# Performance work log

Hardware: AMD Instinct MI355X
Metric: run time of the kernel (lower is better)

Reference implementation:

```python
import jax, jax.numpy as jnp
import numpy as np
from jax import lax

B, C, H, W = 4096, 10, 30, 30
NCOL = C - 1                      # non-background colors 1..9
_pi, _pj = np.triu_indices(NCOL, 1)  # lexicographic (i<j) pair order, matches the python double loop
PI = jnp.asarray(_pi); PJ = jnp.asarray(_pj)
NPAIR = int(_pi.shape[0])         # 36
W_TRANSFORM, W_EXACT, W_AFFINE, W_ROT, W_REFL, W_GEO, W_EDGE, W_CBAL = 0.2, 7.0, 0.4, 0.3, 0.3, 0.5, 0.3, 0.2
GAMMA = 1.4


def setup_inputs() -> dict:
    key = jax.random.key(0)
    ks = jax.random.split(key, 6)
    pred = jax.random.normal(ks[0], (B, C, H, W), jnp.float32)
    tidx = jax.random.randint(ks[1], (B, H, W), 0, C)
    target = jnp.transpose(jax.nn.one_hot(tidx, C, dtype=jnp.float32), (0, 3, 1, 2))
    iidx = jax.random.randint(ks[2], (B, H, W), 0, C)
    input_grid = jnp.transpose(jax.nn.one_hot(iidx, C, dtype=jnp.float32), (0, 3, 1, 2))
    theta = 0.1 * jax.random.normal(ks[3], (B, 2, 3), jnp.float32)
    rot = jax.random.normal(ks[4], (B, 8), jnp.float32)
    refl = jax.random.normal(ks[5], (B, 4), jnp.float32)
    return {"pred_output": pred, "target_output": target, "input_grid": input_grid,
            "theta": theta, "rotation_logits": rot, "reflection_logits": refl}


def _detect_edges(idx):
    # idx: [B,H,W] int; pixel is an edge if it differs from any h/w neighbor
    dh = idx[:, 1:, :] != idx[:, :-1, :]
    dw = idx[:, :, 1:] != idx[:, :, :-1]
    e = jnp.pad(dh, ((0, 0), (1, 0), (0, 0))) | jnp.pad(dh, ((0, 0), (0, 1), (0, 0)))
    e = e | jnp.pad(dw, ((0, 0), (0, 0), (1, 0))) | jnp.pad(dw, ((0, 0), (0, 0), (0, 1)))
    return e


def _entropy_mean(logits):
    lp = jax.nn.log_softmax(logits, axis=1)
    return (-(jnp.exp(lp) * lp).sum(axis=1)).mean()


def _sobel(idx_f):
    sx = jnp.array([[-1., 0., 1.], [-2., 0., 2.], [-1., 0., 1.]], jnp.float32).reshape(1, 1, 3, 3)
    sy = jnp.array([[-1., -2., -1.], [0., 0., 0.], [1., 2., 1.]], jnp.float32).reshape(1, 1, 3, 3)
    x = idx_f[:, None]  # [B,1,H,W]
    dn = ('NCHW', 'OIHW', 'NCHW')
    ex = lax.conv_general_dilated(x, sx, (1, 1), ((1, 1), (1, 1)), dimension_numbers=dn)
    ey = lax.conv_general_dilated(x, sy, (1, 1), ((1, 1), (1, 1)), dimension_numbers=dn)
    return jnp.sqrt(ex * ex + ey * ey)


def _centers(grid):
    # grid: [H,W] int -> per-color (1..9) center of mass and presence
    cols = jnp.arange(1, C)
    mask = (grid[None] == cols[:, None, None]).astype(jnp.float32)  # [9,H,W]
    cnt = mask.sum((1, 2))
    ys = jnp.arange(H, dtype=jnp.float32)[:, None]
    xs = jnp.arange(W, dtype=jnp.float32)[None, :]
    cy = (mask * ys).sum((1, 2)) / jnp.maximum(cnt, 1.0)
    cx = (mask * xs).sum((1, 2)) / jnp.maximum(cnt, 1.0)
    return cy, cx, cnt > 0


def _compact_dists(cy, cx, present):
    # distances for all 36 color pairs, compacted so valid pairs occupy
    # the leading slots in the same lexicographic order as the torch loops
    d = jnp.sqrt((cy[PI] - cy[PJ]) ** 2 + (cx[PI] - cx[PJ]) ** 2)
    v = present[PI] & present[PJ]
    rank = jnp.cumsum(v.astype(jnp.int32)) - 1
    slot = jnp.where(v, rank, NPAIR)          # dump invalid pairs in scratch slot
    compact = jnp.zeros(NPAIR + 1, jnp.float32).at[slot].set(d)
    return compact[:NPAIR], v.sum()


def _geo_sample(pidx, tidx):
    cyp, cxp, prp = _centers(pidx)
    cyt, cxt, prt = _centers(tidx)
    dp, n_p = _compact_dists(cyp, cxp, prp)
    dt, n_t = _compact_dists(cyt, cxt, prt)
    m = jnp.minimum(n_p, n_t)                 # min_len truncation
    use = jnp.arange(NPAIR) < m
    sq = jnp.where(use, (dp - dt) ** 2, 0.0)
    return jnp.where(m > 0, sq.sum() / jnp.maximum(m, 1).astype(jnp.float32), 0.0)


def _components(pred, target, inp, theta, rot, refl):
    tidx = jnp.argmax(target, axis=1)
    pidx = jnp.argmax(pred, axis=1)
    iidx = jnp.argmax(inp, axis=1)
    # spatial focal CE with edge-weighted pixels
    lp = jax.nn.log_softmax(pred, axis=1)
    ce = -jnp.take_along_axis(lp, tidx[:, None], axis=1)[:, 0]  # [B,H,W]
    pt = jnp.exp(-ce)
    sw = jnp.where(_detect_edges(tidx), 1.5, 1.0)
    spatial_focal = ((1.0 - pt) ** GAMMA * ce * sw).mean()
    # exact match bonus / copy penalty
    exact = jnp.all(pidx == tidx, axis=(1, 2)).astype(jnp.float32)
    exact_count = exact.sum()
    exact_bonus = -exact.mean() * W_EXACT
    copy = jnp.all(pidx == iidx, axis=(1, 2)).astype(jnp.float32)
    transform = copy.mean() * W_TRANSFORM
    # affine regularization on theta
    scale_reg = jnp.sqrt((theta[:, :2, :2] ** 2).sum((1, 2)))
    trans_reg = jnp.sqrt((theta[:, :, 2] ** 2).sum(1))
    affine = (scale_reg.mean() + 0.1 * trans_reg.mean()) * W_AFFINE
    rotation = _entropy_mean(rot) * W_ROT
    reflection = _entropy_mean(refl) * W_REFL
    # geometric color-center consistency (vmapped over batch)
    geo = jax.vmap(_geo_sample)(pidx, tidx).sum() / B * W_GEO
    # sobel edge MSE on argmax indices
    pe = _sobel(pidx.astype(jnp.float32))
    te = _sobel(tidx.astype(jnp.float32))
    edge = jnp.mean((pe - te) ** 2) * W_EDGE
    # color balance
    pc = jax.nn.softmax(pred, axis=1).sum((2, 3))
    tc = target.sum((2, 3))
    pc = pc / (pc.sum(1, keepdims=True) + 1e-8)
    tc = tc / (tc.sum(1, keepdims=True) + 1e-8)
    cbal = jnp.mean((pc - tc) ** 2) * W_CBAL
    total = (spatial_focal + transform + affine + rotation + reflection
             + geo + edge + cbal + exact_bonus)
    return (total, spatial_focal, transform, exact_bonus, exact_count,
            affine, rotation, reflection, geo, edge, cbal)


def reference(pred_output, target_output, input_grid, theta, rotation_logits, reflection_logits):
    return _components(pred_output, target_output, input_grid, theta,
                       rotation_logits, reflection_logits)
```

## Files before the change

### kernel.cpp

```cpp
#include <hip/hip_runtime.h>
#include <stdint.h>

#define B_   4096
#define C_   10
#define H_   30
#define W_   30
#define HW_  900
#define NCOL_ 9
#define NPART 9


__device__ __forceinline__ float entropyN(const float* __restrict__ x, int n) {
    float m = x[0];
    for (int i = 1; i < n; ++i) m = fmaxf(m, x[i]);
    float se = 0.f;
    for (int i = 0; i < n; ++i) se += __expf(x[i] - m);
    float lse = m + __logf(se);
    float ent = 0.f;
    for (int i = 0; i < n; ++i) { float lp = x[i] - lse; ent -= __expf(lp) * lp; }
    return ent;
}


__global__ __launch_bounds__(64) void zero_out_k(float* out, int n) {
    int i = threadIdx.x;
    if (i < n) out[i] = 0.f;
}

__global__ __launch_bounds__(256, 4) void loss_main(
    const float* __restrict__ pred, const float* __restrict__ target,
    const float* __restrict__ inp,  const float* __restrict__ theta,
    const float* __restrict__ rotl, const float* __restrict__ refl,
    float* __restrict__ partials ,
    float* __restrict__ out)
{
    __shared__ uint8_t s_t[33 * 32];
    __shared__ uint8_t s_p[33 * 32];
    __shared__ __align__(16) float s_cef[30 * 36];
    __shared__ unsigned long long s_ctr[2][NCOL_];
    __shared__ float s_wred[4][16];
    __shared__ float s_dp[36], s_dt[36];
    __shared__ float s_cy[2][NCOL_], s_cx[2][NCOL_];
    __shared__ int   s_pr[2][NCOL_];
    __shared__ int   s_tcnt[NCOL_];
    __shared__ float s_small[4];

    const int t = threadIdx.x;
    const int b = blockIdx.x;
    const size_t base = (size_t)b * (C_ * HW_);

    float pc[C_];
#pragma unroll
    for (int c = 0; c < C_; ++c) pc[c] = 0.f;
    float exact_f = 1.f, copy_f = 1.f;

    if (t < 225) {
        const int p0 = 4 * t;
        const float* pp = pred   + base + p0;
        const float* tp = target + base + p0;
        const float* gp = inp    + base + p0;

        float4 pfv[C_];
#pragma unroll
        for (int c = 0; c < C_; ++c)
            pfv[c] = *reinterpret_cast<const float4*>(pp + c * HW_);
        float4 tfv[C_];
#pragma unroll
        for (int c = 0; c < C_; ++c)
            tfv[c] = *reinterpret_cast<const float4*>(tp + c * HW_);

        float vt[4]  = {0.f, 0.f, 0.f, 0.f};
        float tif[4] = {0.f, 0.f, 0.f, 0.f};
        float iif[4] = {0.f, 0.f, 0.f, 0.f};
#pragma unroll
        for (int c = 0; c < C_; ++c) {
            float4 gf = *reinterpret_cast<const float4*>(gp + c * HW_);
            const float4 tf = tfv[c];
            const float4 pf = pfv[c];
            const float fc = (float)c;
            vt[0] = fmaf(tf.x, pf.x, vt[0]); vt[1] = fmaf(tf.y, pf.y, vt[1]);
            vt[2] = fmaf(tf.z, pf.z, vt[2]); vt[3] = fmaf(tf.w, pf.w, vt[3]);
            tif[0] = fmaf(tf.x, fc, tif[0]); tif[1] = fmaf(tf.y, fc, tif[1]);
            tif[2] = fmaf(tf.z, fc, tif[2]); tif[3] = fmaf(tf.w, fc, tif[3]);
            iif[0] = fmaf(gf.x, fc, iif[0]); iif[1] = fmaf(gf.y, fc, iif[1]);
            iif[2] = fmaf(gf.z, fc, iif[2]); iif[3] = fmaf(gf.w, fc, iif[3]);
        }

        int h = p0 / 30;
        int w = p0 - 30 * h;
#pragma unroll
        for (int j = 0; j < 4; ++j) {
            const int ti = (int)tif[j];
            const int ii = (int)iif[j];
            const float* pj = (const float*)&pfv[0];
            float pm = pj[j]; int pi = 0;
            float se = 0.f;
            float ex[C_];
#pragma unroll
            for (int c = 0; c < C_; ++c) {
                const float raw = ((const float*)&pfv[c])[j];
                if (c > 0 && raw > pm) { pm = raw; pi = c; }
                float e = __expf(raw);
                ex[c] = e;
                se += e;
            }
            const float inv = __builtin_amdgcn_rcpf(se);
#pragma unroll
            for (int c = 0; c < C_; ++c) pc[c] = fmaf(ex[c], inv, pc[c]);
            const float ce = __logf(se) - vt[j];

            s_t[(h + 1) * 32 + (w + 1)] = (uint8_t)ti;
            s_p[(h + 1) * 32 + (w + 1)] = (uint8_t)pi;
            s_cef[36 * h + w] = ce;
            if (pi != ti) exact_f = 0.f;
            if (pi != ii) copy_f = 0.f;
            if (++w == 30) { w = 0; ++h; }
        }
    } else if (t < 252) {
        const int z = t - 225;
        for (int k = z; k < 32; k += 27) {
            const int g = k >> 4, r = (k >> 3) & 1, dw = k & 7;
            uint32_t* pb = (uint32_t*)((g ? s_p : s_t) + (r ? 31 * 32 : 0));
            pb[dw] = 0u;
        }
        for (int k = z; k < 120; k += 27) {
            const int g = (k >= 60);
            const int kk = k - 60 * g;
            const int r = 1 + (kk >> 1);
            const int cp = (kk & 1) ? 31 : 0;
            (g ? s_p : s_t)[r * 32 + cp] = 0;
        }
        for (int k = z; k < 2 * NCOL_; k += 27) ((unsigned long long*)s_ctr)[k] = 0ull;
    } else if (t == 252) {
        s_small[0] = entropyN(rotl + (size_t)b * 8, 8);
    } else if (t == 253) {
        s_small[1] = entropyN(refl + (size_t)b * 4, 4);
    } else if (t == 254) {
        const float* th = theta + (size_t)b * 6;
        float sreg = sqrtf(th[0]*th[0] + th[1]*th[1] + th[3]*th[3] + th[4]*th[4]);
        float treg = sqrtf(th[2]*th[2] + th[5]*th[5]);
        s_small[2] = sreg + 0.1f * treg;
    }
    __syncthreads();

    float focal = 0.f, edg = 0.f;
    if (t < 240) {
        const int h = t >> 3, wq = t & 7;
        const int w0 = 4 * wq;
        const int npx = (w0 < 28) ? 4 : 2;

        const uint32_t* tr0 = (const uint32_t*)(s_t + 32 * h);
        const uint32_t* tr1 = (const uint32_t*)(s_t + 32 * (h + 1));
        const uint32_t* tr2 = (const uint32_t*)(s_t + 32 * (h + 2));
        const uint32_t* pr0 = (const uint32_t*)(s_p + 32 * h);
        const uint32_t* pr1 = (const uint32_t*)(s_p + 32 * (h + 1));
        const uint32_t* pr2 = (const uint32_t*)(s_p + 32 * (h + 2));

        uint32_t td[3][2] = {{tr0[wq], tr0[wq + 1]}, {tr1[wq], tr1[wq + 1]}, {tr2[wq], tr2[wq + 1]}};
        uint32_t pd[3][2] = {{pr0[wq], pr0[wq + 1]}, {pr1[wq], pr1[wq + 1]}, {pr2[wq], pr2[wq + 1]}};
        const float4 cef = *reinterpret_cast<const float4*>(s_cef + 36 * h + w0);
        const float cearr[4] = {cef.x, cef.y, cef.z, cef.w};

        int tb[3][6], pb[3][6];
#pragma unroll
        for (int r = 0; r < 3; ++r) {
            const uint32_t d0t = td[r][0], d1t = td[r][1];
            tb[r][0] = d0t & 255; tb[r][1] = (d0t >> 8) & 255; tb[r][2] = (d0t >> 16) & 255;
            tb[r][3] = d0t >> 24; tb[r][4] = d1t & 255; tb[r][5] = (d1t >> 8) & 255;
            const uint32_t d0p = pd[r][0], d1p = pd[r][1];
            pb[r][0] = d0p & 255; pb[r][1] = (d0p >> 8) & 255; pb[r][2] = (d0p >> 16) & 255;
            pb[r][3] = d0p >> 24; pb[r][4] = d1p & 255; pb[r][5] = (d1p >> 8) & 255;
        }
        int s1t[6], s2t[6], s1p[6], s2p[6];
#pragma unroll
        for (int j = 0; j < 6; ++j) {
            s1t[j] = tb[0][j] + 2 * tb[1][j] + tb[2][j];
            s2t[j] = tb[2][j] - tb[0][j];
            s1p[j] = pb[0][j] + 2 * pb[1][j] + pb[2][j];
            s2p[j] = pb[2][j] - pb[0][j];
        }
#pragma unroll
        for (int k = 0; k < 4; ++k) {
            if (k < npx) {
                const int w = w0 + k;
                const int tv = tb[1][k + 1], pv = pb[1][k + 1];
                const bool eg = (h > 0  && tb[0][k + 1] != tv) ||
                                (h < 29 && tb[2][k + 1] != tv) ||
                                (w > 0  && tb[1][k]     != tv) ||
                                (w < 29 && tb[1][k + 2] != tv);
                const float ce = cearr[k];
                const float pt = __expf(-ce);
                const float omt = fmaxf(1.f - pt, 0.f);
                focal += __powf(omt, 1.4f) * ce * (eg ? 1.5f : 1.0f);

                const int ext = s1t[k + 2] - s1t[k];
                const int eyt = s2t[k] + 2 * s2t[k + 1] + s2t[k + 2];
                const int exq = s1p[k + 2] - s1p[k];
                const int eyq = s2p[k] + 2 * s2p[k + 1] + s2p[k + 2];
                const float mt = sqrtf((float)(ext * ext + eyt * eyt));
                const float mp = sqrtf((float)(exq * exq + eyq * eyq));
                const float dd = mp - mt;
                edg += dd * dd;

                const unsigned long long add =
                    (1ull << 42) | ((unsigned long long)(unsigned)h << 21) | (unsigned)w;
                if (tv > 0) atomicAdd(&s_ctr[1][tv - 1], add);
                if (pv > 0) atomicAdd(&s_ctr[0][pv - 1], add);
            }
        }
    }

    float vals[14];
    vals[0] = focal; vals[1] = edg;
#pragma unroll
    for (int c = 0; c < C_; ++c) vals[2 + c] = pc[c];
    vals[12] = exact_f; vals[13] = copy_f;
#pragma unroll
    for (int off = 32; off > 0; off >>= 1) {
#pragma unroll
        for (int k = 0; k < 12; ++k) vals[k] += __shfl_down(vals[k], off);
        vals[12] = fminf(vals[12], __shfl_down(vals[12], off));
        vals[13] = fminf(vals[13], __shfl_down(vals[13], off));
    }
    const int wid = t >> 6, lane = t & 63;
    if (lane == 0) {
#pragma unroll
        for (int k = 0; k < 14; ++k) s_wred[wid][k] = vals[k];
    }
    __syncthreads();

    if (t < 18) {
        const int g = (t >= 9);
        const int k = t - 9 * g;
        const unsigned long long q = s_ctr[g][k];
        const int sx = (int)(q & 0x1FFFFF), sy = (int)((q >> 21) & 0x1FFFFF), cn = (int)(q >> 42);
        const float dn = fmaxf((float)cn, 1.f);
        s_cy[g][k] = (float)sy / dn;
        s_cx[g][k] = (float)sx / dn;
        s_pr[g][k] = (cn > 0);
        if (g) s_tcnt[k] = cn;
    }
    __syncthreads();

    if (t < 64) {
        const int l = t;
        const int i = (l >= 8) + (l >= 15) + (l >= 21) + (l >= 26) +
                      (l >= 30) + (l >= 33) + (l >= 35);
        const int j = l - (i * (17 - i)) / 2 + i + 1;
        bool vp = false, vtp = false;
        float dp = 0.f, dt = 0.f;
        if (l < 36) {
            vp  = s_pr[0][i] && s_pr[0][j];
            vtp = s_pr[1][i] && s_pr[1][j];
            float dyp = s_cy[0][i] - s_cy[0][j], dxp = s_cx[0][i] - s_cx[0][j];
            dp = sqrtf(dyp * dyp + dxp * dxp);
            float dyt = s_cy[1][i] - s_cy[1][j], dxt = s_cx[1][i] - s_cx[1][j];
            dt = sqrtf(dyt * dyt + dxt * dxt);
        }
        const unsigned long long mp_mask = __ballot(vp);
        const unsigned long long mt_mask = __ballot(vtp);
        const unsigned long long below = (1ull << l) - 1ull;
        if (vp)  s_dp[__popcll(mp_mask & below)] = dp;
        if (vtp) s_dt[__popcll(mt_mask & below)] = dt;
        const int np = (int)__popcll(mp_mask);
        const int nt = (int)__popcll(mt_mask);
        const int mm = np < nt ? np : nt;
        float term = 0.f;
        if (l < mm) { float d = s_dp[l] - s_dt[l]; term = d * d; }
#pragma unroll
        for (int off = 32; off > 0; off >>= 1) term += __shfl_down(term, off);

        if (t == 0) {
            const float geo_b = (mm > 0) ? term / (float)mm : 0.f;

            float r[14];
#pragma unroll
            for (int k = 0; k < 14; ++k) r[k] = s_wred[0][k];
            for (int w2 = 1; w2 < 4; ++w2) {
#pragma unroll
                for (int k = 0; k < 12; ++k) r[k] += s_wred[w2][k];
                r[12] = fminf(r[12], s_wred[w2][12]);
                r[13] = fminf(r[13], s_wred[w2][13]);
            }

            float pcs = 0.f;
#pragma unroll
            for (int c = 0; c < C_; ++c) pcs += r[2 + c];
            const float ipcs = 1.f / (pcs + 1e-8f);
            int tsum = 0;
#pragma unroll
            for (int k = 0; k < NCOL_; ++k) tsum += s_tcnt[k];
            float cb = 0.f;
            const float itd = 1.f / (900.f + 1e-8f);
            {
                float d = r[2] * ipcs - (float)(HW_ - tsum) * itd;
                cb += d * d;
            }
#pragma unroll
            for (int c = 1; c < C_; ++c) {
                float d = r[2 + c] * ipcs - (float)s_tcnt[c - 1] * itd;
                cb += d * d;
            }

            float res[NPART];
            res[0] = r[0];
            res[1] = r[12];
            res[2] = r[13];
            res[3] = s_small[2];
            res[4] = s_small[0];
            res[5] = s_small[1];
            res[6] = geo_b;
            res[7] = r[1];
            res[8] = cb;

            if (partials) {
                float* pw = partials + (size_t)b * NPART;
#pragma unroll
                for (int k = 0; k < NPART; ++k) pw[k] = res[k];
            } else {
                atomicAdd(&out[1],  res[0]);
                atomicAdd(&out[2],  res[2]);
                atomicAdd(&out[4],  res[1]);
                atomicAdd(&out[5],  res[3]);
                atomicAdd(&out[6],  res[4]);
                atomicAdd(&out[7],  res[5]);
                atomicAdd(&out[8],  res[6]);
                atomicAdd(&out[9],  res[7]);
                atomicAdd(&out[10], res[8]);
            }
        }
    }
}

__device__ __forceinline__ void write_final(float* out,
    double focal_s, double exact_s, double copy_s, double aff_s,
    double rot_s, double refl_s, double geo_s, double edge_s, double cbal_s)
{
    const double invB = 1.0 / (double)B_;
    float focal      = (float)(focal_s / ((double)B_ * (double)HW_));
    float transform  = (float)(copy_s * invB * 0.2);
    float exact_cnt  = (float)exact_s;
    float exact_bns  = (float)(-(exact_s * invB) * 7.0);
    float affine     = (float)(aff_s * invB * 0.4);
    float rotation   = (float)(rot_s * invB * 0.3);
    float reflection = (float)(refl_s * invB * 0.3);
    float geo        = (float)(geo_s * invB * 0.5);
    float edge       = (float)(edge_s / ((double)B_ * (double)HW_) * 0.3);
    float cbal       = (float)(cbal_s / ((double)B_ * (double)C_) * 0.2);
    out[0] = focal + transform + affine + rotation + reflection + geo + edge + cbal + exact_bns;
    out[1] = focal; out[2] = transform; out[3] = exact_bns; out[4] = exact_cnt;
    out[5] = affine; out[6] = rotation; out[7] = reflection; out[8] = geo;
    out[9] = edge; out[10] = cbal;
}

__global__ __launch_bounds__(256) void reduce_partials(
    const float* __restrict__ partials, float* __restrict__ out)
{
    __shared__ double sh[256][NPART];
    const int t = threadIdx.x;
    double acc[NPART];
#pragma unroll
    for (int k = 0; k < NPART; ++k) acc[k] = 0.0;
    for (int b = t; b < B_; b += 256) {
        const float* pp = partials + (size_t)b * NPART;
#pragma unroll
        for (int k = 0; k < NPART; ++k) acc[k] += (double)pp[k];
    }
#pragma unroll
    for (int k = 0; k < NPART; ++k) sh[t][k] = acc[k];
    __syncthreads();
    for (int s = 128; s > 0; s >>= 1) {
        if (t < s) {
#pragma unroll
            for (int k = 0; k < NPART; ++k) sh[t][k] += sh[t + s][k];
        }
        __syncthreads();
    }
    if (t == 0) {
        write_final(out, sh[0][0], sh[0][1], sh[0][2], sh[0][3],
                    sh[0][4], sh[0][5], sh[0][6], sh[0][7], sh[0][8]);
    }
}

__global__ void finalize_atomic(float* out) {
    if (threadIdx.x == 0) {
        write_final(out, (double)out[1], (double)out[4], (double)out[2], (double)out[5],
                    (double)out[6], (double)out[7], (double)out[8], (double)out[9],
                    (double)out[10]);
    }
}


extern "C" void kernel_launch(void* const* d_in, const int* in_sizes, int n_in,
                              void* d_out, int out_size, void* d_ws, size_t ws_size,
                              hipStream_t stream) {
    const float* pred   = (const float*)d_in[0];
    const float* target = (const float*)d_in[1];
    const float* inp    = (const float*)d_in[2];
    const float* theta  = (const float*)d_in[3];
    const float* rotl   = (const float*)d_in[4];
    const float* refl   = (const float*)d_in[5];
    float* out = (float*)d_out;

    const size_t need = (size_t)B_ * NPART * sizeof(float);
    if (d_ws != nullptr && ws_size >= need) {
        loss_main<<<B_, 256, 0, stream>>>(pred, target, inp, theta, rotl, refl,
                                          (float*)d_ws, out);
        reduce_partials<<<1, 256, 0, stream>>>((const float*)d_ws, out);
    } else {
        zero_out_k<<<1, 64, 0, stream>>>(out, out_size);
        loss_main<<<B_, 256, 0, stream>>>(pred, target, inp, theta, rotl, refl,
                                          nullptr, out);
        finalize_atomic<<<1, 1, 0, stream>>>(out);
    }
}
```

Before: 94.75 us.

## Process one batch sample per wavefront instead of per block

Remaps the loss kernel so each 64-lane wavefront handles one sample, with four samples per 256-thread block. All block-wide __syncthreads are replaced by wave-local LDS fences, exact and copy flags become wave votes, and the cross-wave shared-memory reduction is dropped. Focal weighting is also precomputed per pixel in the first pass, so the edge pass only adds the extra half weight on edge pixels. Each wave now loops over four chunks of pixels serially, which lowers memory-level parallelism per sample and raises LDS use per block in exchange for removing block barriers.

Measured after the change: 98.55 us. +4.0%, slower.

```diff
diff --git a/kernel.cpp b/kernel.cpp
--- a/kernel.cpp
+++ b/kernel.cpp
@@ -8,6 +8,7 @@
 #define HW_  900
 #define NCOL_ 9
 #define NPART 9
+#define WVB  4
 
 
 __device__ __forceinline__ float entropyN(const float* __restrict__ x, int n) {
@@ -21,6 +22,12 @@
     return ent;
 }
 
+__device__ __forceinline__ void wave_fence_lds() {
+    asm volatile("s_waitcnt lgkmcnt(0)" ::: "memory");
+    __builtin_amdgcn_wave_barrier();
+    __builtin_amdgcn_sched_barrier(0);
+}
+
 
 __global__ __launch_bounds__(64) void zero_out_k(float* out, int n) {
     int i = threadIdx.x;
@@ -34,132 +41,130 @@
     float* __restrict__ partials ,
     float* __restrict__ out)
 {
-    __shared__ uint8_t s_t[33 * 32];
-    __shared__ uint8_t s_p[33 * 32];
-    __shared__ __align__(16) float s_cef[30 * 36];
-    __shared__ unsigned long long s_ctr[2][NCOL_];
-    __shared__ float s_wred[4][16];
-    __shared__ float s_dp[36], s_dt[36];
-    __shared__ float s_cy[2][NCOL_], s_cx[2][NCOL_];
-    __shared__ int   s_pr[2][NCOL_];
-    __shared__ int   s_tcnt[NCOL_];
-    __shared__ float s_small[4];
-
-    const int t = threadIdx.x;
-    const int b = blockIdx.x;
+    __shared__ uint8_t s_t[WVB][33 * 32];
+    __shared__ uint8_t s_p[WVB][33 * 32];
+    __shared__ __align__(16) float s_fb[WVB][30 * 36];
+    __shared__ unsigned long long s_ctr[WVB][2][NCOL_];
+    __shared__ float s_cy[WVB][2][NCOL_], s_cx[WVB][2][NCOL_];
+    __shared__ int   s_pr[WVB][2][NCOL_];
+    __shared__ int   s_tcnt[WVB][NCOL_];
+    __shared__ float s_dp[WVB][36], s_dt[WVB][36];
+    __shared__ float s_small[WVB][4];
+
+    const int t    = threadIdx.x;
+    const int wv   = t >> 6;
+    const int lane = t & 63;
+    const int b    = blockIdx.x * WVB + wv;
     const size_t base = (size_t)b * (C_ * HW_);
 
+    uint8_t* st = s_t[wv];
+    uint8_t* sp = s_p[wv];
+    float*   sfb = s_fb[wv];
+
+    {
+        uint32_t* zt = (uint32_t*)st;
+        uint32_t* zp = (uint32_t*)sp;
+#pragma unroll 1
+        for (int k = lane; k < 264; k += 64) { zt[k] = 0u; zp[k] = 0u; }
+        if (lane < 2 * NCOL_) ((unsigned long long*)s_ctr[wv])[lane] = 0ull;
+    }
+    wave_fence_lds();
+
     float pc[C_];
 #pragma unroll
     for (int c = 0; c < C_; ++c) pc[c] = 0.f;
-    float exact_f = 1.f, copy_f = 1.f;
-
-    if (t < 225) {
-        const int p0 = 4 * t;
-        const float* pp = pred   + base + p0;
-        const float* tp = target + base + p0;
-        const float* gp = inp    + base + p0;
-
-        float4 pfv[C_];
-#pragma unroll
-        for (int c = 0; c < C_; ++c)
-            pfv[c] = *reinterpret_cast<const float4*>(pp + c * HW_);
-        float4 tfv[C_];
-#pragma unroll
-        for (int c = 0; c < C_; ++c)
-            tfv[c] = *reinterpret_cast<const float4*>(tp + c * HW_);
-
-        float vt[4]  = {0.f, 0.f, 0.f, 0.f};
-        float tif[4] = {0.f, 0.f, 0.f, 0.f};
-        float iif[4] = {0.f, 0.f, 0.f, 0.f};
-#pragma unroll
-        for (int c = 0; c < C_; ++c) {
-            float4 gf = *reinterpret_cast<const float4*>(gp + c * HW_);
-            const float4 tf = tfv[c];
-            const float4 pf = pfv[c];
-            const float fc = (float)c;
-            vt[0] = fmaf(tf.x, pf.x, vt[0]); vt[1] = fmaf(tf.y, pf.y, vt[1]);
-            vt[2] = fmaf(tf.z, pf.z, vt[2]); vt[3] = fmaf(tf.w, pf.w, vt[3]);
-            tif[0] = fmaf(tf.x, fc, tif[0]); tif[1] = fmaf(tf.y, fc, tif[1]);
-            tif[2] = fmaf(tf.z, fc, tif[2]); tif[3] = fmaf(tf.w, fc, tif[3]);
-            iif[0] = fmaf(gf.x, fc, iif[0]); iif[1] = fmaf(gf.y, fc, iif[1]);
-            iif[2] = fmaf(gf.z, fc, iif[2]); iif[3] = fmaf(gf.w, fc, iif[3]);
-        }
-
-        int h = p0 / 30;
-        int w = p0 - 30 * h;
-#pragma unroll
-        for (int j = 0; j < 4; ++j) {
-            const int ti = (int)tif[j];
-            const int ii = (int)iif[j];
-            const float* pj = (const float*)&pfv[0];
-            float pm = pj[j]; int pi = 0;
-            float se = 0.f;
-            float ex[C_];
+    float focal_base = 0.f;
+    bool ok_e = true, ok_c = true;
+
+#pragma unroll 1
+    for (int it = 0; it < 4; ++it) {
+        const int p0 = 256 * it + 4 * lane;
+        if (p0 < HW_) {
+            const float* pp = pred   + base + p0;
+            const float* tp = target + base + p0;
+            const float* gp = inp    + base + p0;
+
+            float4 pfv[C_];
+#pragma unroll
+            for (int c = 0; c < C_; ++c)
+                pfv[c] = *reinterpret_cast<const float4*>(pp + c * HW_);
+            float4 tfv[C_];
+#pragma unroll
+            for (int c = 0; c < C_; ++c)
+                tfv[c] = *reinterpret_cast<const float4*>(tp + c * HW_);
+
+            float vt[4]  = {0.f, 0.f, 0.f, 0.f};
+            float tif[4] = {0.f, 0.f, 0.f, 0.f};
+            float iif[4] = {0.f, 0.f, 0.f, 0.f};
 #pragma unroll
             for (int c = 0; c < C_; ++c) {
-                const float raw = ((const float*)&pfv[c])[j];
-                if (c > 0 && raw > pm) { pm = raw; pi = c; }
-                float e = __expf(raw);
-                ex[c] = e;
-                se += e;
+                float4 gf = *reinterpret_cast<const float4*>(gp + c * HW_);
+                const float4 tf = tfv[c];
+                const float4 pf = pfv[c];
+                const float fc = (float)c;
+                vt[0] = fmaf(tf.x, pf.x, vt[0]); vt[1] = fmaf(tf.y, pf.y, vt[1]);
+                vt[2] = fmaf(tf.z, pf.z, vt[2]); vt[3] = fmaf(tf.w, pf.w, vt[3]);
+                tif[0] = fmaf(tf.x, fc, tif[0]); tif[1] = fmaf(tf.y, fc, tif[1]);
+                tif[2] = fmaf(tf.z, fc, tif[2]); tif[3] = fmaf(tf.w, fc, tif[3]);
+                iif[0] = fmaf(gf.x, fc, iif[0]); iif[1] = fmaf(gf.y, fc, iif[1]);
+                iif[2] = fmaf(gf.z, fc, iif[2]); iif[3] = fmaf(gf.w, fc, iif[3]);
             }
-            const float inv = __builtin_amdgcn_rcpf(se);
-#pragma unroll
-            for (int c = 0; c < C_; ++c) pc[c] = fmaf(ex[c], inv, pc[c]);
-            const float ce = __logf(se) - vt[j];
-
-            s_t[(h + 1) * 32 + (w + 1)] = (uint8_t)ti;
-            s_p[(h + 1) * 32 + (w + 1)] = (uint8_t)pi;
-            s_cef[36 * h + w] = ce;
-            if (pi != ti) exact_f = 0.f;
-            if (pi != ii) copy_f = 0.f;
-            if (++w == 30) { w = 0; ++h; }
-        }
-    } else if (t < 252) {
-        const int z = t - 225;
-        for (int k = z; k < 32; k += 27) {
-            const int g = k >> 4, r = (k >> 3) & 1, dw = k & 7;
-            uint32_t* pb = (uint32_t*)((g ? s_p : s_t) + (r ? 31 * 32 : 0));
-            pb[dw] = 0u;
-        }
-        for (int k = z; k < 120; k += 27) {
-            const int g = (k >= 60);
-            const int kk = k - 60 * g;
-            const int r = 1 + (kk >> 1);
-            const int cp = (kk & 1) ? 31 : 0;
-            (g ? s_p : s_t)[r * 32 + cp] = 0;
-        }
-        for (int k = z; k < 2 * NCOL_; k += 27) ((unsigned long long*)s_ctr)[k] = 0ull;
-    } else if (t == 252) {
-        s_small[0] = entropyN(rotl + (size_t)b * 8, 8);
-    } else if (t == 253) {
-        s_small[1] = entropyN(refl + (size_t)b * 4, 4);
-    } else if (t == 254) {
-        const float* th = theta + (size_t)b * 6;
-        float sreg = sqrtf(th[0]*th[0] + th[1]*th[1] + th[3]*th[3] + th[4]*th[4]);
-        float treg = sqrtf(th[2]*th[2] + th[5]*th[5]);
-        s_small[2] = sreg + 0.1f * treg;
-    }
-    __syncthreads();
-
-    float focal = 0.f, edg = 0.f;
-    if (t < 240) {
-        const int h = t >> 3, wq = t & 7;
+
+            int h = p0 / 30;
+            int w = p0 - 30 * h;
+#pragma unroll
+            for (int j = 0; j < 4; ++j) {
+                const int ti = (int)tif[j];
+                const int ii = (int)iif[j];
+                float pm = ((const float*)&pfv[0])[j]; int pi = 0;
+                float se = 0.f;
+                float ex[C_];
+#pragma unroll
+                for (int c = 0; c < C_; ++c) {
+                    const float raw = ((const float*)&pfv[c])[j];
+                    if (c > 0 && raw > pm) { pm = raw; pi = c; }
+                    float e = __expf(raw);
+                    ex[c] = e;
+                    se += e;
+                }
+                const float inv = __builtin_amdgcn_rcpf(se);
+#pragma unroll
+                for (int c = 0; c < C_; ++c) pc[c] = fmaf(ex[c], inv, pc[c]);
+                const float ce = __logf(se) - vt[j];
+                const float pt = __expf(-ce);
+                const float omt = fmaxf(1.f - pt, 0.f);
+                const float fb = __powf(omt, 1.4f) * ce;
+                focal_base += fb;
+
+                st[(h + 1) * 32 + (w + 1)] = (uint8_t)ti;
+                sp[(h + 1) * 32 + (w + 1)] = (uint8_t)pi;
+                sfb[36 * h + w] = fb;
+                if (pi != ti) ok_e = false;
+                if (pi != ii) ok_c = false;
+                if (++w == 30) { w = 0; ++h; }
+            }
+        }
+    }
+    wave_fence_lds();
+
+    float edg = 0.f, focal_edge = 0.f;
+#pragma unroll 1
+    for (int s = lane; s < 240; s += 64) {
+        const int h = s >> 3, wq = s & 7;
         const int w0 = 4 * wq;
         const int npx = (w0 < 28) ? 4 : 2;
 
-        const uint32_t* tr0 = (const uint32_t*)(s_t + 32 * h);
-        const uint32_t* tr1 = (const uint32_t*)(s_t + 32 * (h + 1));
-        const uint32_t* tr2 = (const uint32_t*)(s_t + 32 * (h + 2));
-        const uint32_t* pr0 = (const uint32_t*)(s_p + 32 * h);
-        const uint32_t* pr1 = (const uint32_t*)(s_p + 32 * (h + 1));
-        const uint32_t* pr2 = (const uint32_t*)(s_p + 32 * (h + 2));
+        const uint32_t* tr0 = (const uint32_t*)(st + 32 * h);
+        const uint32_t* tr1 = (const uint32_t*)(st + 32 * (h + 1));
+        const uint32_t* tr2 = (const uint32_t*)(st + 32 * (h + 2));
+        const uint32_t* pr0 = (const uint32_t*)(sp + 32 * h);
+        const uint32_t* pr1 = (const uint32_t*)(sp + 32 * (h + 1));
+        const uint32_t* pr2 = (const uint32_t*)(sp + 32 * (h + 2));
 
         uint32_t td[3][2] = {{tr0[wq], tr0[wq + 1]}, {tr1[wq], tr1[wq + 1]}, {tr2[wq], tr2[wq + 1]}};
         uint32_t pd[3][2] = {{pr0[wq], pr0[wq + 1]}, {pr1[wq], pr1[wq + 1]}, {pr2[wq], pr2[wq + 1]}};
-        const float4 cef = *reinterpret_cast<const float4*>(s_cef + 36 * h + w0);
-        const float cearr[4] = {cef.x, cef.y, cef.z, cef.w};
+        const float4 fbf = *reinterpret_cast<const float4*>(sfb + 36 * h + w0);
+        const float fbarr[4] = {fbf.x, fbf.y, fbf.z, fbf.w};
 
         int tb[3][6], pb[3][6];
 #pragma unroll
@@ -188,10 +193,7 @@
                                 (h < 29 && tb[2][k + 1] != tv) ||
                                 (w > 0  && tb[1][k]     != tv) ||
                                 (w < 29 && tb[1][k + 2] != tv);
-                const float ce = cearr[k];
-                const float pt = __expf(-ce);
-                const float omt = fmaxf(1.f - pt, 0.f);
-                focal += __powf(omt, 1.4f) * ce * (eg ? 1.5f : 1.0f);
+                if (eg) focal_edge += fbarr[k];
 
                 const int ext = s1t[k + 2] - s1t[k];
                 const int eyt = s2t[k] + 2 * s2t[k + 1] + s2t[k + 2];
@@ -204,130 +206,125 @@
 
                 const unsigned long long add =
                     (1ull << 42) | ((unsigned long long)(unsigned)h << 21) | (unsigned)w;
-                if (tv > 0) atomicAdd(&s_ctr[1][tv - 1], add);
-                if (pv > 0) atomicAdd(&s_ctr[0][pv - 1], add);
+                if (tv > 0) atomicAdd(&s_ctr[wv][1][tv - 1], add);
+                if (pv > 0) atomicAdd(&s_ctr[wv][0][pv - 1], add);
             }
         }
     }
 
-    float vals[14];
-    vals[0] = focal; vals[1] = edg;
+    float vals[12];
+    vals[0] = focal_base + 0.5f * focal_edge;
+    vals[1] = edg;
 #pragma unroll
     for (int c = 0; c < C_; ++c) vals[2 + c] = pc[c];
-    vals[12] = exact_f; vals[13] = copy_f;
 #pragma unroll
     for (int off = 32; off > 0; off >>= 1) {
 #pragma unroll
         for (int k = 0; k < 12; ++k) vals[k] += __shfl_down(vals[k], off);
-        vals[12] = fminf(vals[12], __shfl_down(vals[12], off));
-        vals[13] = fminf(vals[13], __shfl_down(vals[13], off));
-    }
-    const int wid = t >> 6, lane = t & 63;
-    if (lane == 0) {
-#pragma unroll
-        for (int k = 0; k < 14; ++k) s_wred[wid][k] = vals[k];
-    }
-    __syncthreads();
-
-    if (t < 18) {
-        const int g = (t >= 9);
-        const int k = t - 9 * g;
-        const unsigned long long q = s_ctr[g][k];
+    }
+    const float exact_f = __all(ok_e) ? 1.f : 0.f;
+    const float copy_f  = __all(ok_c) ? 1.f : 0.f;
+
+    if (lane == 1)      s_small[wv][0] = entropyN(rotl + (size_t)b * 8, 8);
+    else if (lane == 2) s_small[wv][1] = entropyN(refl + (size_t)b * 4, 4);
+    else if (lane == 3) {
+        const float* th = theta + (size_t)b * 6;
+        float sreg = sqrtf(th[0]*th[0] + th[1]*th[1] + th[3]*th[3] + th[4]*th[4]);
+        float treg = sqrtf(th[2]*th[2] + th[5]*th[5]);
+        s_small[wv][2] = sreg + 0.1f * treg;
+    }
+
+    wave_fence_lds();
+    if (lane < 18) {
+        const int g = (lane >= 9);
+        const int k = lane - 9 * g;
+        const unsigned long long q = s_ctr[wv][g][k];
         const int sx = (int)(q & 0x1FFFFF), sy = (int)((q >> 21) & 0x1FFFFF), cn = (int)(q >> 42);
         const float dn = fmaxf((float)cn, 1.f);
-        s_cy[g][k] = (float)sy / dn;
-        s_cx[g][k] = (float)sx / dn;
-        s_pr[g][k] = (cn > 0);
-        if (g) s_tcnt[k] = cn;
-    }
-    __syncthreads();
-
-    if (t < 64) {
-        const int l = t;
-        const int i = (l >= 8) + (l >= 15) + (l >= 21) + (l >= 26) +
-                      (l >= 30) + (l >= 33) + (l >= 35);
-        const int j = l - (i * (17 - i)) / 2 + i + 1;
-        bool vp = false, vtp = false;
-        float dp = 0.f, dt = 0.f;
-        if (l < 36) {
-            vp  = s_pr[0][i] && s_pr[0][j];
-            vtp = s_pr[1][i] && s_pr[1][j];
-            float dyp = s_cy[0][i] - s_cy[0][j], dxp = s_cx[0][i] - s_cx[0][j];
-            dp = sqrtf(dyp * dyp + dxp * dxp);
-            float dyt = s_cy[1][i] - s_cy[1][j], dxt = s_cx[1][i] - s_cx[1][j];
-            dt = sqrtf(dyt * dyt + dxt * dxt);
-        }
-        const unsigned long long mp_mask = __ballot(vp);
-        const unsigned long long mt_mask = __ballot(vtp);
-        const unsigned long long below = (1ull << l) - 1ull;
-        if (vp)  s_dp[__popcll(mp_mask & below)] = dp;
-        if (vtp) s_dt[__popcll(mt_mask & below)] = dt;
-        const int np = (int)__popcll(mp_mask);
-        const int nt = (int)__popcll(mt_mask);
-        const int mm = np < nt ? np : nt;
-        float term = 0.f;
-        if (l < mm) { float d = s_dp[l] - s_dt[l]; term = d * d; }
-#pragma unroll
-        for (int off = 32; off > 0; off >>= 1) term += __shfl_down(term, off);
-
-        if (t == 0) {
-            const float geo_b = (mm > 0) ? term / (float)mm : 0.f;
-
-            float r[14];
-#pragma unroll
-            for (int k = 0; k < 14; ++k) r[k] = s_wred[0][k];
-            for (int w2 = 1; w2 < 4; ++w2) {
-#pragma unroll
-                for (int k = 0; k < 12; ++k) r[k] += s_wred[w2][k];
-                r[12] = fminf(r[12], s_wred[w2][12]);
-                r[13] = fminf(r[13], s_wred[w2][13]);
-            }
-
-            float pcs = 0.f;
-#pragma unroll
-            for (int c = 0; c < C_; ++c) pcs += r[2 + c];
-            const float ipcs = 1.f / (pcs + 1e-8f);
-            int tsum = 0;
-#pragma unroll
-            for (int k = 0; k < NCOL_; ++k) tsum += s_tcnt[k];
-            float cb = 0.f;
-            const float itd = 1.f / (900.f + 1e-8f);
-            {
-                float d = r[2] * ipcs - (float)(HW_ - tsum) * itd;
-                cb += d * d;
-            }
-#pragma unroll
-            for (int c = 1; c < C_; ++c) {
-                float d = r[2 + c] * ipcs - (float)s_tcnt[c - 1] * itd;
-                cb += d * d;
-            }
-
-            float res[NPART];
-            res[0] = r[0];
-            res[1] = r[12];
-            res[2] = r[13];
-            res[3] = s_small[2];
-            res[4] = s_small[0];
-            res[5] = s_small[1];
-            res[6] = geo_b;
-            res[7] = r[1];
-            res[8] = cb;
-
-            if (partials) {
-                float* pw = partials + (size_t)b * NPART;
-#pragma unroll
-                for (int k = 0; k < NPART; ++k) pw[k] = res[k];
-            } else {
-                atomicAdd(&out[1],  res[0]);
-                atomicAdd(&out[2],  res[2]);
-                atomicAdd(&out[4],  res[1]);
-                atomicAdd(&out[5],  res[3]);
-                atomicAdd(&out[6],  res[4]);
-                atomicAdd(&out[7],  res[5]);
-                atomicAdd(&out[8],  res[6]);
-                atomicAdd(&out[9],  res[7]);
-                atomicAdd(&out[10], res[8]);
-            }
+        s_cy[wv][g][k] = (float)sy / dn;
+        s_cx[wv][g][k] = (float)sx / dn;
+        s_pr[wv][g][k] = (cn > 0);
+        if (g) s_tcnt[wv][k] = cn;
+    }
+    wave_fence_lds();
+
+    const int l = lane;
+    const int i = (l >= 8) + (l >= 15) + (l >= 21) + (l >= 26) +
+                  (l >= 30) + (l >= 33) + (l >= 35);
+    const int j = l - (i * (17 - i)) / 2 + i + 1;
+    bool vp = false, vtp = false;
+    float dp = 0.f, dt = 0.f;
+    if (l < 36) {
+        vp  = s_pr[wv][0][i] && s_pr[wv][0][j];
+        vtp = s_pr[wv][1][i] && s_pr[wv][1][j];
+        float dyp = s_cy[wv][0][i] - s_cy[wv][0][j], dxp = s_cx[wv][0][i] - s_cx[wv][0][j];
+        dp = sqrtf(dyp * dyp + dxp * dxp);
+        float dyt = s_cy[wv][1][i] - s_cy[wv][1][j], dxt = s_cx[wv][1][i] - s_cx[wv][1][j];
+        dt = sqrtf(dyt * dyt + dxt * dxt);
+    }
+    const unsigned long long mp_mask = __ballot(vp);
+    const unsigned long long mt_mask = __ballot(vtp);
+    const unsigned long long below = (1ull << l) - 1ull;
+    if (vp)  s_dp[wv][__popcll(mp_mask & below)] = dp;
+    if (vtp) s_dt[wv][__popcll(mt_mask & below)] = dt;
+    const int np = (int)__popcll(mp_mask);
+    const int nt = (int)__popcll(mt_mask);
+    const int mm = np < nt ? np : nt;
+    wave_fence_lds();
+    float term = 0.f;
+    if (l < mm) { float d = s_dp[wv][l] - s_dt[wv][l]; term = d * d; }
+#pragma unroll
+    for (int off = 32; off > 0; off >>= 1) term += __shfl_down(term, off);
+
+    wave_fence_lds();
+
+    if (lane == 0) {
+        const float geo_b = (mm > 0) ? term / (float)mm : 0.f;
+
+        float pcs = 0.f;
+#pragma unroll
+        for (int c = 0; c < C_; ++c) pcs += vals[2 + c];
+        const float ipcs = 1.f / (pcs + 1e-8f);
+        int tsum = 0;
+#pragma unroll
+        for (int k = 0; k < NCOL_; ++k) tsum += s_tcnt[wv][k];
+        float cb = 0.f;
+        const float itd = 1.f / (900.f + 1e-8f);
+        {
+            float d = vals[2] * ipcs - (float)(HW_ - tsum) * itd;
+            cb += d * d;
+        }
+#pragma unroll
+        for (int c = 1; c < C_; ++c) {
+            float d = vals[2 + c] * ipcs - (float)s_tcnt[wv][c - 1] * itd;
+            cb += d * d;
+        }
+
+        float res[NPART];
+        res[0] = vals[0];
+        res[1] = exact_f;
+        res[2] = copy_f;
+        res[3] = s_small[wv][2];
+        res[4] = s_small[wv][0];
+        res[5] = s_small[wv][1];
+        res[6] = geo_b;
+        res[7] = vals[1];
+        res[8] = cb;
+
+        if (partials) {
+            float* pw = partials + (size_t)b * NPART;
+#pragma unroll
+            for (int k = 0; k < NPART; ++k) pw[k] = res[k];
+        } else {
+            atomicAdd(&out[1],  res[0]);
+            atomicAdd(&out[2],  res[2]);
+            atomicAdd(&out[4],  res[1]);
+            atomicAdd(&out[5],  res[3]);
+            atomicAdd(&out[6],  res[4]);
+            atomicAdd(&out[7],  res[5]);
+            atomicAdd(&out[8],  res[6]);
+            atomicAdd(&out[9],  res[7]);
+            atomicAdd(&out[10], res[8]);
         }
     }
 }
@@ -404,13 +401,13 @@
 
     const size_t need = (size_t)B_ * NPART * sizeof(float);
     if (d_ws != nullptr && ws_size >= need) {
-        loss_main<<<B_, 256, 0, stream>>>(pred, target, inp, theta, rotl, refl,
-                                          (float*)d_ws, out);
+        loss_main<<<B_ / WVB, 256, 0, stream>>>(pred, target, inp, theta, rotl, refl,
+                                                (float*)d_ws, out);
         reduce_partials<<<1, 256, 0, stream>>>((const float*)d_ws, out);
     } else {
         zero_out_k<<<1, 64, 0, stream>>>(out, out_size);
-        loss_main<<<B_, 256, 0, stream>>>(pred, target, inp, theta, rotl, refl,
-                                          nullptr, out);
+        loss_main<<<B_ / WVB, 256, 0, stream>>>(pred, target, inp, theta, rotl, refl,
+                                                nullptr, out);
         finalize_atomic<<<1, 1, 0, stream>>>(out);
     }
 }
```

## Stage inputs through double-buffered async global-to-LDS loads in pixel tiles

Applied to the files above, without the earlier changes.

Replaces the per-thread float4 register loads of pred, target and input with a four-tile loop. Each tile is copied straight into a double-buffered shared-memory area with global_load_lds, and explicit vmcnt waits and barriers let the next tile's copy overlap the current tile's softmax and argmax work. The focal base term now runs in the first phase, and the edge pass adds only the extra 0.5 weight for edge pixels. The aim is to overlap memory traffic with compute, but the new staging buffer takes about 60KB of LDS per block, which can lower occupancy on a kernel that is already close to its bandwidth limit.

Result: slower. 134.7 us (+42.2%).

```diff
diff --git a/kernel.cpp b/kernel.cpp
--- a/kernel.cpp
+++ b/kernel.cpp
@@ -8,6 +8,11 @@
 #define HW_  900
 #define NCOL_ 9
 #define NPART 9
+#define TILE 256
+#define NT   4
+
+#define AS1 __attribute__((address_space(1)))
+#define AS3 __attribute__((address_space(3)))
 
 
 __device__ __forceinline__ float entropyN(const float* __restrict__ x, int n) {
@@ -34,9 +39,10 @@
     float* __restrict__ partials ,
     float* __restrict__ out)
 {
+    __shared__ float s_buf[2][3][C_][TILE];
     __shared__ uint8_t s_t[33 * 32];
     __shared__ uint8_t s_p[33 * 32];
-    __shared__ __align__(16) float s_cef[30 * 36];
+    __shared__ __align__(16) float s_fb[30 * 36];
     __shared__ unsigned long long s_ctr[2][NCOL_];
     __shared__ float s_wred[4][16];
     __shared__ float s_dp[36], s_dt[36];
@@ -45,61 +51,79 @@
     __shared__ int   s_tcnt[NCOL_];
     __shared__ float s_small[4];
 
-    const int t = threadIdx.x;
-    const int b = blockIdx.x;
+    const int t    = threadIdx.x;
+    const int wid  = t >> 6;
+    const int lane = t & 63;
+    const int b    = blockIdx.x;
     const size_t base = (size_t)b * (C_ * HW_);
 
+    {
+        uint32_t* zt = (uint32_t*)s_t;
+        uint32_t* zp = (uint32_t*)s_p;
+        for (int k = t; k < 264; k += 256) { zt[k] = 0u; zp[k] = 0u; }
+        if (t < 2 * NCOL_) ((unsigned long long*)s_ctr)[t] = 0ull;
+    }
+    __syncthreads();
+
+    const size_t LIM = (size_t)B_ * C_ * HW_ - 4;
+    auto stage = [&](int tb, int tile, bool clampT) {
+        const size_t toff = base + (size_t)tile * TILE + 4 * (size_t)lane;
+#pragma unroll 1
+        for (int ch = wid; ch < C_; ch += 4) {
+            size_t idx = toff + (size_t)ch * HW_;
+            if (clampT && idx > LIM) idx = LIM;
+            __builtin_amdgcn_global_load_lds((const AS1 void*)(pred + idx),
+                                             (AS3 void*)&s_buf[tb][0][ch][0], 16, 0, 0);
+            __builtin_amdgcn_global_load_lds((const AS1 void*)(target + idx),
+                                             (AS3 void*)&s_buf[tb][1][ch][0], 16, 0, 0);
+            __builtin_amdgcn_global_load_lds((const AS1 void*)(inp + idx),
+                                             (AS3 void*)&s_buf[tb][2][ch][0], 16, 0, 0);
+        }
+    };
+
     float pc[C_];
 #pragma unroll
     for (int c = 0; c < C_; ++c) pc[c] = 0.f;
-    float exact_f = 1.f, copy_f = 1.f;
-
-    if (t < 225) {
-        const int p0 = 4 * t;
-        const float* pp = pred   + base + p0;
-        const float* tp = target + base + p0;
-        const float* gp = inp    + base + p0;
-
-        float4 pfv[C_];
-#pragma unroll
-        for (int c = 0; c < C_; ++c)
-            pfv[c] = *reinterpret_cast<const float4*>(pp + c * HW_);
-        float4 tfv[C_];
-#pragma unroll
-        for (int c = 0; c < C_; ++c)
-            tfv[c] = *reinterpret_cast<const float4*>(tp + c * HW_);
-
-        float vt[4]  = {0.f, 0.f, 0.f, 0.f};
-        float tif[4] = {0.f, 0.f, 0.f, 0.f};
-        float iif[4] = {0.f, 0.f, 0.f, 0.f};
-#pragma unroll
-        for (int c = 0; c < C_; ++c) {
-            float4 gf = *reinterpret_cast<const float4*>(gp + c * HW_);
-            const float4 tf = tfv[c];
-            const float4 pf = pfv[c];
-            const float fc = (float)c;
-            vt[0] = fmaf(tf.x, pf.x, vt[0]); vt[1] = fmaf(tf.y, pf.y, vt[1]);
-            vt[2] = fmaf(tf.z, pf.z, vt[2]); vt[3] = fmaf(tf.w, pf.w, vt[3]);
-            tif[0] = fmaf(tf.x, fc, tif[0]); tif[1] = fmaf(tf.y, fc, tif[1]);
-            tif[2] = fmaf(tf.z, fc, tif[2]); tif[3] = fmaf(tf.w, fc, tif[3]);
-            iif[0] = fmaf(gf.x, fc, iif[0]); iif[1] = fmaf(gf.y, fc, iif[1]);
-            iif[2] = fmaf(gf.z, fc, iif[2]); iif[3] = fmaf(gf.w, fc, iif[3]);
-        }
-
-        int h = p0 / 30;
-        int w = p0 - 30 * h;
-#pragma unroll
-        for (int j = 0; j < 4; ++j) {
-            const int ti = (int)tif[j];
-            const int ii = (int)iif[j];
-            const float* pj = (const float*)&pfv[0];
-            float pm = pj[j]; int pi = 0;
-            float se = 0.f;
+    float focal_base = 0.f;
+    bool ok_e = true, ok_c = true;
+
+    stage(0, 0, false);
+#pragma unroll 1
+    for (int tt = 0; tt < NT; ++tt) {
+        const int tb = tt & 1;
+        if (tt + 1 < NT) {
+            stage(tb ^ 1, tt + 1, (tt + 1 == NT - 1));
+            if (wid < 2) asm volatile("s_waitcnt vmcnt(9)" ::: "memory");
+            else         asm volatile("s_waitcnt vmcnt(6)" ::: "memory");
+        } else {
+            asm volatile("s_waitcnt vmcnt(0)" ::: "memory");
+        }
+        __builtin_amdgcn_s_barrier();
+        asm volatile("" ::: "memory");
+
+        const int px = tt * TILE + t;
+        if (px < HW_) {
+            const float* bp  = &s_buf[tb][0][0][t];
+            const float* btg = &s_buf[tb][1][0][t];
+            const float* big = &s_buf[tb][2][0][t];
+            float tif = 0.f, iif = 0.f;
+            float pv[C_];
+#pragma unroll
+            for (int c = 0; c < C_; ++c) {
+                pv[c] = bp[c * TILE];
+                tif = fmaf(btg[c * TILE], (float)c, tif);
+                iif = fmaf(big[c * TILE], (float)c, iif);
+            }
+            const int ti = (int)tif;
+            const int ii = (int)iif;
+            float pm = pv[0]; int pi = 0;
+            float se = 0.f, vt = pv[0];
             float ex[C_];
 #pragma unroll
             for (int c = 0; c < C_; ++c) {
-                const float raw = ((const float*)&pfv[c])[j];
+                const float raw = pv[c];
                 if (c > 0 && raw > pm) { pm = raw; pi = c; }
+                if (c == ti) vt = raw;
                 float e = __expf(raw);
                 ex[c] = e;
                 se += e;
@@ -107,30 +131,86 @@
             const float inv = __builtin_amdgcn_rcpf(se);
 #pragma unroll
             for (int c = 0; c < C_; ++c) pc[c] = fmaf(ex[c], inv, pc[c]);
-            const float ce = __logf(se) - vt[j];
-
+            const float ce = __logf(se) - vt;
+            const float pt = __expf(-ce);
+            const float omt = fmaxf(1.f - pt, 0.f);
+            const float fb = __powf(omt, 1.4f) * ce;
+            focal_base += fb;
+
+            const int h = px / 30, w = px - 30 * h;
             s_t[(h + 1) * 32 + (w + 1)] = (uint8_t)ti;
             s_p[(h + 1) * 32 + (w + 1)] = (uint8_t)pi;
-            s_cef[36 * h + w] = ce;
-            if (pi != ti) exact_f = 0.f;
-            if (pi != ii) copy_f = 0.f;
-            if (++w == 30) { w = 0; ++h; }
-        }
-    } else if (t < 252) {
-        const int z = t - 225;
-        for (int k = z; k < 32; k += 27) {
-            const int g = k >> 4, r = (k >> 3) & 1, dw = k & 7;
-            uint32_t* pb = (uint32_t*)((g ? s_p : s_t) + (r ? 31 * 32 : 0));
-            pb[dw] = 0u;
-        }
-        for (int k = z; k < 120; k += 27) {
-            const int g = (k >= 60);
-            const int kk = k - 60 * g;
-            const int r = 1 + (kk >> 1);
-            const int cp = (kk & 1) ? 31 : 0;
-            (g ? s_p : s_t)[r * 32 + cp] = 0;
-        }
-        for (int k = z; k < 2 * NCOL_; k += 27) ((unsigned long long*)s_ctr)[k] = 0ull;
+            s_fb[36 * h + w] = fb;
+            if (pi != ti) ok_e = false;
+            if (pi != ii) ok_c = false;
+        }
+        asm volatile("s_waitcnt lgkmcnt(0)" ::: "memory");
+        __builtin_amdgcn_s_barrier();
+        asm volatile("" ::: "memory");
+    }
+
+    float focal_edge = 0.f, edg = 0.f;
+    if (t < 240) {
+        const int h = t >> 3, wq = t & 7;
+        const int w0 = 4 * wq;
+        const int npx = (w0 < 28) ? 4 : 2;
+
+        const uint32_t* tr0 = (const uint32_t*)(s_t + 32 * h);
+        const uint32_t* tr1 = (const uint32_t*)(s_t + 32 * (h + 1));
+        const uint32_t* tr2 = (const uint32_t*)(s_t + 32 * (h + 2));
+        const uint32_t* pr0 = (const uint32_t*)(s_p + 32 * h);
+        const uint32_t* pr1 = (const uint32_t*)(s_p + 32 * (h + 1));
+        const uint32_t* pr2 = (const uint32_t*)(s_p + 32 * (h + 2));
+
+        uint32_t td[3][2] = {{tr0[wq], tr0[wq + 1]}, {tr1[wq], tr1[wq + 1]}, {tr2[wq], tr2[wq + 1]}};
+        uint32_t pd[3][2] = {{pr0[wq], pr0[wq + 1]}, {pr1[wq], pr1[wq + 1]}, {pr2[wq], pr2[wq + 1]}};
+        const float4 fbf = *reinterpret_cast<const float4*>(s_fb + 36 * h + w0);
+        const float fbarr[4] = {fbf.x, fbf.y, fbf.z, fbf.w};
+
+        int tb2[3][6], pb2[3][6];
+#pragma unroll
+        for (int r = 0; r < 3; ++r) {
+            const uint32_t d0t = td[r][0], d1t = td[r][1];
+            tb2[r][0] = d0t & 255; tb2[r][1] = (d0t >> 8) & 255; tb2[r][2] = (d0t >> 16) & 255;
+            tb2[r][3] = d0t >> 24; tb2[r][4] = d1t & 255; tb2[r][5] = (d1t >> 8) & 255;
+            const uint32_t d0p = pd[r][0], d1p = pd[r][1];
+            pb2[r][0] = d0p & 255; pb2[r][1] = (d0p >> 8) & 255; pb2[r][2] = (d0p >> 16) & 255;
+            pb2[r][3] = d0p >> 24; pb2[r][4] = d1p & 255; pb2[r][5] = (d1p >> 8) & 255;
+        }
+        int s1t[6], s2t[6], s1p[6], s2p[6];
+#pragma unroll
+        for (int j = 0; j < 6; ++j) {
+            s1t[j] = tb2[0][j] + 2 * tb2[1][j] + tb2[2][j];
+            s2t[j] = tb2[2][j] - tb2[0][j];
+            s1p[j] = pb2[0][j] + 2 * pb2[1][j] + pb2[2][j];
+            s2p[j] = pb2[2][j] - pb2[0][j];
+        }
+#pragma unroll
+        for (int k = 0; k < 4; ++k) {
+            if (k < npx) {
+                const int w = w0 + k;
+                const int tv = tb2[1][k + 1], pv2 = pb2[1][k + 1];
+                const bool eg = (h > 0  && tb2[0][k + 1] != tv) ||
+                                (h < 29 && tb2[2][k + 1] != tv) ||
+                                (w > 0  && tb2[1][k]     != tv) ||
+                                (w < 29 && tb2[1][k + 2] != tv);
+                if (eg) focal_edge += fbarr[k];
+
+                const int ext = s1t[k + 2] - s1t[k];
+                const int eyt = s2t[k] + 2 * s2t[k + 1] + s2t[k + 2];
+                const int exq = s1p[k + 2] - s1p[k];
+                const int eyq = s2p[k] + 2 * s2p[k + 1] + s2p[k + 2];
+                const float mt = sqrtf((float)(ext * ext + eyt * eyt));
+                const float mp = sqrtf((float)(exq * exq + eyq * eyq));
+                const float dd = mp - mt;
+                edg += dd * dd;
+
+                const unsigned long long add =
+                    (1ull << 42) | ((unsigned long long)(unsigned)h << 21) | (unsigned)w;
+                if (tv  > 0) atomicAdd(&s_ctr[1][tv  - 1], add);
+                if (pv2 > 0) atomicAdd(&s_ctr[0][pv2 - 1], add);
+            }
+        }
     } else if (t == 252) {
         s_small[0] = entropyN(rotl + (size_t)b * 8, 8);
     } else if (t == 253) {
@@ -141,80 +221,14 @@
         float treg = sqrtf(th[2]*th[2] + th[5]*th[5]);
         s_small[2] = sreg + 0.1f * treg;
     }
-    __syncthreads();
-
-    float focal = 0.f, edg = 0.f;
-    if (t < 240) {
-        const int h = t >> 3, wq = t & 7;
-        const int w0 = 4 * wq;
-        const int npx = (w0 < 28) ? 4 : 2;
-
-        const uint32_t* tr0 = (const uint32_t*)(s_t + 32 * h);
-        const uint32_t* tr1 = (const uint32_t*)(s_t + 32 * (h + 1));
-        const uint32_t* tr2 = (const uint32_t*)(s_t + 32 * (h + 2));
-        const uint32_t* pr0 = (const uint32_t*)(s_p + 32 * h);
-        const uint32_t* pr1 = (const uint32_t*)(s_p + 32 * (h + 1));
-        const uint32_t* pr2 = (const uint32_t*)(s_p + 32 * (h + 2));
-
-        uint32_t td[3][2] = {{tr0[wq], tr0[wq + 1]}, {tr1[wq], tr1[wq + 1]}, {tr2[wq], tr2[wq + 1]}};
-        uint32_t pd[3][2] = {{pr0[wq], pr0[wq + 1]}, {pr1[wq], pr1[wq + 1]}, {pr2[wq], pr2[wq + 1]}};
-        const float4 cef = *reinterpret_cast<const float4*>(s_cef + 36 * h + w0);
-        const float cearr[4] = {cef.x, cef.y, cef.z, cef.w};
-
-        int tb[3][6], pb[3][6];
-#pragma unroll
-        for (int r = 0; r < 3; ++r) {
-            const uint32_t d0t = td[r][0], d1t = td[r][1];
-            tb[r][0] = d0t & 255; tb[r][1] = (d0t >> 8) & 255; tb[r][2] = (d0t >> 16) & 255;
-            tb[r][3] = d0t >> 24; tb[r][4] = d1t & 255; tb[r][5] = (d1t >> 8) & 255;
-            const uint32_t d0p = pd[r][0], d1p = pd[r][1];
-            pb[r][0] = d0p & 255; pb[r][1] = (d0p >> 8) & 255; pb[r][2] = (d0p >> 16) & 255;
-            pb[r][3] = d0p >> 24; pb[r][4] = d1p & 255; pb[r][5] = (d1p >> 8) & 255;
-        }
-        int s1t[6], s2t[6], s1p[6], s2p[6];
-#pragma unroll
-        for (int j = 0; j < 6; ++j) {
-            s1t[j] = tb[0][j] + 2 * tb[1][j] + tb[2][j];
-            s2t[j] = tb[2][j] - tb[0][j];
-            s1p[j] = pb[0][j] + 2 * pb[1][j] + pb[2][j];
-            s2p[j] = pb[2][j] - pb[0][j];
-        }
-#pragma unroll
-        for (int k = 0; k < 4; ++k) {
-            if (k < npx) {
-                const int w = w0 + k;
-                const int tv = tb[1][k + 1], pv = pb[1][k + 1];
-                const bool eg = (h > 0  && tb[0][k + 1] != tv) ||
-                                (h < 29 && tb[2][k + 1] != tv) ||
-                                (w > 0  && tb[1][k]     != tv) ||
-                                (w < 29 && tb[1][k + 2] != tv);
-                const float ce = cearr[k];
-                const float pt = __expf(-ce);
-                const float omt = fmaxf(1.f - pt, 0.f);
-                focal += __powf(omt, 1.4f) * ce * (eg ? 1.5f : 1.0f);
-
-                const int ext = s1t[k + 2] - s1t[k];
-                const int eyt = s2t[k] + 2 * s2t[k + 1] + s2t[k + 2];
-                const int exq = s1p[k + 2] - s1p[k];
-                const int eyq = s2p[k] + 2 * s2p[k + 1] + s2p[k + 2];
-                const float mt = sqrtf((float)(ext * ext + eyt * eyt));
-                const float mp = sqrtf((float)(exq * exq + eyq * eyq));
-                const float dd = mp - mt;
-                edg += dd * dd;
-
-                const unsigned long long add =
-                    (1ull << 42) | ((unsigned long long)(unsigned)h << 21) | (unsigned)w;
-                if (tv > 0) atomicAdd(&s_ctr[1][tv - 1], add);
-                if (pv > 0) atomicAdd(&s_ctr[0][pv - 1], add);
-            }
-        }
-    }
 
     float vals[14];
-    vals[0] = focal; vals[1] = edg;
+    vals[0] = focal_base + 0.5f * focal_edge;
+    vals[1] = edg;
 #pragma unroll
     for (int c = 0; c < C_; ++c) vals[2 + c] = pc[c];
-    vals[12] = exact_f; vals[13] = copy_f;
+    vals[12] = ok_e ? 1.f : 0.f;
+    vals[13] = ok_c ? 1.f : 0.f;
 #pragma unroll
     for (int off = 32; off > 0; off >>= 1) {
 #pragma unroll
@@ -222,7 +236,6 @@
         vals[12] = fminf(vals[12], __shfl_down(vals[12], off));
         vals[13] = fminf(vals[13], __shfl_down(vals[13], off));
     }
-    const int wid = t >> 6, lane = t & 63;
     if (lane == 0) {
 #pragma unroll
         for (int k = 0; k < 14; ++k) s_wred[wid][k] = vals[k];
@@ -265,6 +278,8 @@
         const int np = (int)__popcll(mp_mask);
         const int nt = (int)__popcll(mt_mask);
         const int mm = np < nt ? np : nt;
+        asm volatile("s_waitcnt lgkmcnt(0)" ::: "memory");
+        __builtin_amdgcn_wave_barrier();
         float term = 0.f;
         if (l < mm) { float d = s_dp[l] - s_dt[l]; term = d * d; }
 #pragma unroll
```
